# Kernel optimization log

Measured on AMD Instinct MI355X. Metric: run time of the kernel, lower is better.

## Reference

```python
import jax, jax.numpy as jnp
import numpy as np

# --- static config (matches init_kwargs) ---
DIM = 192          # kv channels
CS = 2             # channel_scale -> q/out channels = DIM//CS
NH = 6             # num heads
WS = 4             # kv window size (q window = 2*WS)
S, H, W = 16, 32, 32          # coarse (input) resolution
SD, HD, WD = 32, 64, 64
HEAD = DIM // NH
SCALE = HEAD ** -0.5

# Relative position index: query coords are the fine-grid positions mapped to
# coarse coords via repeat_interleave(2) (as in the original coords_s/h/w),
# key coords are the coarse window positions. (Original torch code contained a
# buggy 2D->3D port of the strided key subsample; this is the consistent 3D form.)
_r = np.repeat(np.arange(WS), 2)
qc = np.stack(np.meshgrid(_r, _r, _r, indexing='ij'), -1).reshape(-1, 3)        # (512,3)
_k = np.arange(WS)
kc = np.stack(np.meshgrid(_k, _k, _k, indexing='ij'), -1).reshape(-1, 3)        # (64,3)
_rel = qc[:, None, :] - kc[None, :, :] + (WS - 1)                                # in [0, 2*WS-2]
REL_INDEX = jnp.asarray(_rel[..., 0] * (2 * WS - 1) ** 2 + _rel[..., 1] * (2 * WS - 1) + _rel[..., 2])  # (512,64)
TABLE_ROWS = (4 * WS - 1) ** 3  # as in original parameter shape


def ln(x, g, b, eps=1e-5):
    mu = jnp.mean(x, axis=-1, keepdims=True)
    var = jnp.mean(jnp.square(x - mu), axis=-1, keepdims=True)
    return (x - mu) * jax.lax.rsqrt(var + eps) * g + b


def win_part(x, ws):
    # (B,s,h,w,C) -> (B*num_windows, ws^3, C)
    B, s, h, w, C = x.shape
    x = x.reshape(B, s // ws, ws, h // ws, ws, w // ws, ws, C)
    return x.transpose(0, 1, 3, 5, 2, 4, 6, 7).reshape(-1, ws * ws * ws, C)


def win_rev(x, ws, B, s, h, w):
    # (B*num_windows, ws^3, C) -> (B,s,h,w,C)
    C = x.shape[-1]
    x = x.reshape(B, s // ws, h // ws, w // ws, ws, ws, ws, C)
    return x.transpose(0, 1, 4, 2, 5, 3, 6, 7).reshape(B, s, h, w, C)


def setup_inputs() -> dict:
    key = jax.random.key(0)
    ks = jax.random.split(key, 12)
    d = DIM
    dh = d // CS
    hid = int(dh * 4)
    f = lambda i, shape: jax.random.normal(ks[i], shape, jnp.float32) * 0.02
    return dict(
        x=jax.random.normal(ks[0], (2, S * H * W, d), jnp.float32),
        x_downsampled=jax.random.normal(ks[1], (2, SD * HD * WD, dh), jnp.float32),
        gamma1=jnp.ones((d,), jnp.float32), beta1=jnp.zeros((d,), jnp.float32),
        W_kv=f(2, (d, 2 * d)), b_kv=jnp.zeros((2 * d,), jnp.float32),
        W_q=f(3, (dh, d)), b_q=jnp.zeros((d,), jnp.float32),
        W_proj=f(4, (d, dh)), b_proj=jnp.zeros((dh,), jnp.float32),
        bias_table=f(5, (TABLE_ROWS, NH)),
        exp_gamma=jnp.ones((d,), jnp.float32), exp_beta=jnp.zeros((d,), jnp.float32),
        deconv_w=f(6, (d, dh, 2, 2, 2)), deconv_b=jnp.zeros((dh,), jnp.float32),
        gamma2=jnp.ones((dh,), jnp.float32), beta2=jnp.zeros((dh,), jnp.float32),
        W1=f(7, (dh, hid)), b1=jnp.zeros((hid,), jnp.float32),
        W2=f(8, (hid, dh)), b2=jnp.zeros((dh,), jnp.float32),
        padwh=0,
    )


def reference(x, x_downsampled, gamma1, beta1, W_kv, b_kv, W_q, b_q, W_proj, b_proj,
              bias_table, exp_gamma, exp_beta, deconv_w, deconv_b, gamma2, beta2,
              W1, b1, W2, b2, padwh):
    B = x.shape[0]
    d = DIM
    dh = d // CS
    # ---- windowed cross attention: kv from coarse x (norm1), q from fine skip ----
    kv = ln(x, gamma1, beta1).reshape(B, S, H, W, d)
    kv_w = win_part(kv, WS)                                           # (Bw, 64, d)
    q_w = win_part(x_downsampled.reshape(B, SD, HD, WD, dh), 2 * WS)  # (Bw, 512, dh)
    Bw, N, _ = kv_w.shape
    Nq = q_w.shape[1]
    kvp = kv_w @ W_kv + b_kv                                          # (Bw, N, 2d)
    k, v = jnp.split(kvp, 2, axis=-1)
    k = k.reshape(Bw, N, NH, HEAD).transpose(0, 2, 1, 3)
    v = v.reshape(Bw, N, NH, HEAD).transpose(0, 2, 1, 3)
    q = (q_w @ W_q + b_q).reshape(Bw, Nq, NH, HEAD).transpose(0, 2, 1, 3) * SCALE
    attn = jnp.einsum('bhqd,bhkd->bhqk', q, k)                        # (Bw, NH, 512, 64)
    bias = bias_table[REL_INDEX].transpose(2, 0, 1)                   # (NH, 512, 64)
    attn = jax.nn.softmax(attn + bias[None], axis=-1)
    out = jnp.einsum('bhqk,bhkd->bhqd', attn, v).transpose(0, 2, 1, 3).reshape(Bw, Nq, d)
    out = out @ W_proj + b_proj                                       # (Bw, Nq, dh)
    out = win_rev(out, 2 * WS, B, SD, HD, WD).reshape(B, SD * HD * WD, dh)
    # ---- Patch_Expanding residual: LN + ConvTranspose3d(k=2, s=2) ----
    xe = ln(x, exp_gamma, exp_beta).reshape(B, S, H, W, d)
    sc = jnp.einsum('bshwc,coijk->bsihjwko', xe, deconv_w) + deconv_b  # (B,S,2,H,2,W,2,dh)
    sc = sc.reshape(B, SD * HD * WD, dh)
    # ---- residual + MLP ----
    y = sc + out
    hdn = jax.nn.gelu(ln(y, gamma2, beta2) @ W1 + b1, approximate=False)
    return y + (hdn @ W2 + b2)
```

## Files before the change

### kernel.cpp

```cpp
#include <hip/hip_runtime.h>
#include <math.h>

#define ATT_SCALE 0.17677669529663687f

typedef __bf16 bf16x8 __attribute__((ext_vector_type(8)));
typedef __bf16 bf16x4 __attribute__((ext_vector_type(4)));
typedef float  f32x4  __attribute__((ext_vector_type(4)));

#define MFMA16(a,b,c) __builtin_amdgcn_mfma_f32_16x16x32_bf16(a,b,c,0,0,0)

#define BIAS_BYTES 786432
#define WKV_OFF 0
#define WQ_OFF  73728
#define WP_OFF  92160
#define WD_OFF  110592
#define W1_OFF  258048
#define W2_OFF  294912
#define NSWZ    331776

static __device__ __forceinline__ float gelu_exact(float v){
    return 0.5f * v * (1.0f + erff(v * 0.70710678118654752f));
}

static __device__ __forceinline__ bf16x8 afrag(const __bf16* w, int NRT, int kt, int rt, int lane){
    return ((const bf16x8*)w)[(kt*NRT + rt)*64 + lane];
}

__global__ __launch_bounds__(256) void k_prep(const float* __restrict__ table,
    const float* __restrict__ Wkv, const float* __restrict__ Wq,
    const float* __restrict__ Wp,  const float* __restrict__ Wd,
    const float* __restrict__ W1,  const float* __restrict__ W2,
    float* __restrict__ bias, __bf16* __restrict__ wsw){
    int id = blockIdx.x * 256 + threadIdx.x;
    if (id < 196608){
        int k  = id & 63;
        int qg = (id >> 6) & 511;
        int h  = id >> 15;
        int qi = qg >> 6, qj = (qg >> 3) & 7, qk = qg & 7;
        int ki = k >> 4,  kj = (k >> 2) & 3,  kk = k & 3;
        int r0 = (qi >> 1) - ki + 3;
        int r1 = (qj >> 1) - kj + 3;
        int r2 = (qk >> 1) - kk + 3;
        bias[id] = table[((r0 * 7 + r1) * 7 + r2) * 6 + h];
        return;
    }
    id -= 196608;
    if (id >= NSWZ) return;
    if (id >= WD_OFF && id < W1_OFF){
        int lid  = id - WD_OFF;
        int j    = lid & 7, lane = (lid >> 3) & 63, tile = lid >> 9;
        int rt   = tile % 24;
        int kt2  = tile / 24;
        int ii   = kt2 / 6, kt = kt2 % 6;
        int n    = rt * 16 + (lane & 15);
        int o    = n % 96, jk = n / 96;
        int kdim = kt * 32 + (lane >> 4) * 8 + j;
        wsw[id] = (__bf16)(Wd[(kdim * 96 + o) * 8 + ii * 4 + jk]);
        return;
    }
    const float* W; int N, NRT, off; float sc = 1.f;
    if      (id < WQ_OFF){ W = Wkv; N = 384; NRT = 24; off = WKV_OFF; }
    else if (id < WP_OFF){ W = Wq;  N = 192; NRT = 12; off = WQ_OFF; sc = ATT_SCALE; }
    else if (id < WD_OFF){ W = Wp;  N = 96;  NRT = 6;  off = WP_OFF; }
    else if (id < W2_OFF){ W = W1;  N = 384; NRT = 24; off = W1_OFF; }
    else                 { W = W2;  N = 96;  NRT = 6;  off = W2_OFF; }
    int lid  = id - off;
    int j    = lid & 7, lane = (lid >> 3) & 63, tile = lid >> 9;
    int rt   = tile % NRT, kt = tile / NRT;
    int n    = rt * 16 + (lane & 15);
    int k    = kt * 32 + (lane >> 4) * 8 + j;
    wsw[id + 0] = (__bf16)(W[k * N + n] * sc);
}

__global__ __launch_bounds__(512) void k_deconv(const float* __restrict__ x,
    const float* __restrict__ eg, const float* __restrict__ eb,
    const __bf16* __restrict__ wsw, const float* __restrict__ db,
    float* __restrict__ out){
    __shared__ __bf16 xe[64][200];
    const int tid = threadIdx.x, lane = tid & 63, w = tid >> 6;
    const int ci0 = blockIdx.x * 64;
    {
        int row = tid >> 3, sub = tid & 7;
        const float* xp = x + (ci0 + row) * 192 + sub * 24;
        float v[24]; float s = 0.f, ss = 0.f;
        #pragma unroll
        for (int i = 0; i < 6; i++){
            float4 t = ((const float4*)xp)[i];
            v[4*i] = t.x; v[4*i+1] = t.y; v[4*i+2] = t.z; v[4*i+3] = t.w;
            s += t.x + t.y + t.z + t.w;
            ss += t.x*t.x + t.y*t.y + t.z*t.z + t.w*t.w;
        }
        #pragma unroll
        for (int m = 1; m < 8; m <<= 1){ s += __shfl_xor(s, m); ss += __shfl_xor(ss, m); }
        float mu = s * (1.f/192.f), var = ss * (1.f/192.f) - mu*mu, rs = rsqrtf(var + 1e-5f);
        #pragma unroll
        for (int i = 0; i < 3; i++){
            bf16x8 t;
            #pragma unroll
            for (int jj = 0; jj < 8; jj++){
                int c = sub*24 + 8*i + jj;
                t[jj] = (__bf16)((v[8*i+jj] - mu) * rs * eg[c] + eb[c]);
            }
            *(bf16x8*)&xe[row][sub*24 + 8*i] = t;
        }
    }
    __syncthreads();
    const int li = lane & 15, gt = lane >> 4;
    const int ct = w & 3, ii = w >> 2;
    const int tok = ct * 16 + li;
    const int ci  = ci0 + tok;
    const int bb  = ci >> 14, rem = ci & 16383;
    const int sC  = rem >> 10, hC = (rem >> 5) & 31, wC = rem & 31;
    const int ftb = ((bb * 32 + 2 * sC) * 64 + 2 * hC) * 64 + 2 * wC + ii * 4096;
    bf16x8 bfr[6];
    #pragma unroll
    for (int kt = 0; kt < 6; kt++) bfr[kt] = *(const bf16x8*)&xe[tok][kt*32 + gt*8];
    const __bf16* wd = wsw + WD_OFF + ii * 73728;
    for (int rt = 0; rt < 24; rt++){
        f32x4 acc = {0.f,0.f,0.f,0.f};
        #pragma unroll
        for (int kt = 0; kt < 6; kt++) acc = MFMA16(afrag(wd, 24, kt, rt, lane), bfr[kt], acc);
        int m  = rt * 16 + (gt << 2);
        int jk = m / 96, o = m - jk * 96;
        int ft = ftb + (jk >> 1) * 64 + (jk & 1);
        float4 d4 = *(const float4*)&db[o];
        float4 res;
        res.x = acc[0] + d4.x; res.y = acc[1] + d4.y;
        res.z = acc[2] + d4.z; res.w = acc[3] + d4.w;
        *(float4*)&out[ft * 96 + o] = res;
    }
}

__global__ __launch_bounds__(512) void k_attn(const float* __restrict__ x,
    const float* __restrict__ xd, const float* __restrict__ g1, const float* __restrict__ b1v,
    const float* __restrict__ bkv, const float* __restrict__ bq, const float* __restrict__ bpj,
    const __bf16* __restrict__ wsw, const float* __restrict__ bias, float* __restrict__ yout){
    __shared__ __bf16 Qs[64][196];
    __shared__ __bf16 Os[64][196];
    __shared__ __bf16 Ks[64][196];
    __shared__ __bf16 Vt[192][68];
    const int tid = threadIdx.x, lane = tid & 63, w = tid >> 6;
    const int win = blockIdx.x, b = win >> 8, wrem = win & 255;
    const int sw_ = wrem >> 6, hw_ = (wrem >> 3) & 7, ww_ = wrem & 7;

    {
        int row = tid >> 3, sub = tid & 7;
        int si = row >> 4, hi = (row >> 2) & 3, wi = row & 3;
        int ci = ((b * 16 + 4 * sw_ + si) * 32 + 4 * hw_ + hi) * 32 + 4 * ww_ + wi;
        const float* xp = x + ci * 192 + sub * 24;
        float v[24]; float s = 0.f, ss = 0.f;
        #pragma unroll
        for (int i = 0; i < 6; i++){
            float4 t = ((const float4*)xp)[i];
            v[4*i] = t.x; v[4*i+1] = t.y; v[4*i+2] = t.z; v[4*i+3] = t.w;
            s += t.x + t.y + t.z + t.w;
            ss += t.x*t.x + t.y*t.y + t.z*t.z + t.w*t.w;
        }
        #pragma unroll
        for (int m = 1; m < 8; m <<= 1){ s += __shfl_xor(s, m); ss += __shfl_xor(ss, m); }
        float mu = s * (1.f/192.f), var = ss * (1.f/192.f) - mu*mu, rs = rsqrtf(var + 1e-5f);
        #pragma unroll
        for (int i = 0; i < 3; i++){
            bf16x8 t;
            #pragma unroll
            for (int jj = 0; jj < 8; jj++){
                int c = sub*24 + 8*i + jj;
                t[jj] = (__bf16)((v[8*i+jj] - mu) * rs * g1[c] + b1v[c]);
            }
            *(bf16x8*)&Qs[row][sub*24 + 8*i] = t;
        }
    }
    __syncthreads();
    {
        const int ct = w & 3, rh = w >> 2;
        const int tok = ct * 16 + (lane & 15);
        bf16x8 bfr[6];
        #pragma unroll
        for (int kt = 0; kt < 6; kt++) bfr[kt] = *(const bf16x8*)&Qs[tok][kt*32 + (lane>>4)*8];
        #pragma unroll
        for (int i = 0; i < 12; i++){
            int rt = rh * 12 + i;
            f32x4 acc = {0.f,0.f,0.f,0.f};
            #pragma unroll
            for (int kt = 0; kt < 6; kt++) acc = MFMA16(afrag(wsw + WKV_OFF, 24, kt, rt, lane), bfr[kt], acc);
            int cb = rt * 16 + ((lane >> 4) << 2);
            float4 b4 = *(const float4*)&bkv[cb];
            acc[0] += b4.x; acc[1] += b4.y; acc[2] += b4.z; acc[3] += b4.w;
            if (cb < 192){
                bf16x4 t;
                #pragma unroll
                for (int r = 0; r < 4; r++) t[r] = (__bf16)acc[r];
                *(bf16x4*)&Ks[tok][cb] = t;
            } else {
                #pragma unroll
                for (int r = 0; r < 4; r++) Vt[cb - 192 + r][tok] = (__bf16)acc[r];
            }
        }
    }
    __syncthreads();

    const int li_ = lane & 15, gt_ = lane >> 4, rsel = lane >> 5;
    const int ctQ = w & 3, rhQ = w >> 2;
    const int qlQ = ctQ * 16 + li_;

    auto qproj = [&](int qt){
        const int ft = ((b * 32 + 8 * sw_ + qt) * 64 + 8 * hw_ + (qlQ >> 3)) * 64 + 8 * ww_ + (qlQ & 7);
        bf16x8 bfr[3];
        #pragma unroll
        for (int kt = 0; kt < 3; kt++){
            const float* xp = xd + ft * 96 + kt * 32 + gt_ * 8;
            float4 t0 = *(const float4*)xp;
            float4 t1 = *(const float4*)(xp + 4);
            bf16x8 t;
            t[0]=(__bf16)t0.x; t[1]=(__bf16)t0.y; t[2]=(__bf16)t0.z; t[3]=(__bf16)t0.w;
            t[4]=(__bf16)t1.x; t[5]=(__bf16)t1.y; t[6]=(__bf16)t1.z; t[7]=(__bf16)t1.w;
            bfr[kt] = t;
        }
        #pragma unroll
        for (int i = 0; i < 6; i++){
            int rt = rhQ * 6 + i;
            f32x4 acc = {0.f,0.f,0.f,0.f};
            #pragma unroll
            for (int kt = 0; kt < 3; kt++) acc = MFMA16(afrag(wsw + WQ_OFF, 12, kt, rt, lane), bfr[kt], acc);
            int cb = rt * 16 + (gt_ << 2);
            float4 b4 = *(const float4*)&bq[cb];
            bf16x4 t;
            t[0] = (__bf16)(acc[0] + b4.x * ATT_SCALE);
            t[1] = (__bf16)(acc[1] + b4.y * ATT_SCALE);
            t[2] = (__bf16)(acc[2] + b4.z * ATT_SCALE);
            t[3] = (__bf16)(acc[3] + b4.w * ATT_SCALE);
            *(bf16x4*)&Qs[qlQ][cb] = t;
        }
    };

    auto outproj = [&](int qt){
        const int ft = ((b * 32 + 8 * sw_ + qt) * 64 + 8 * hw_ + (qlQ >> 3)) * 64 + 8 * ww_ + (qlQ & 7);
        bf16x8 bfr[6];
        #pragma unroll
        for (int kt = 0; kt < 6; kt++) bfr[kt] = *(const bf16x8*)&Os[qlQ][kt*32 + gt_*8];
        #pragma unroll
        for (int i = 0; i < 3; i++){
            int rt = rhQ * 3 + i;
            f32x4 acc = {0.f,0.f,0.f,0.f};
            #pragma unroll
            for (int kt = 0; kt < 6; kt++) acc = MFMA16(afrag(wsw + WP_OFF, 6, kt, rt, lane), bfr[kt], acc);
            int cb = rt * 16 + (gt_ << 2);
            float4 b4 = *(const float4*)&bpj[cb];
            float4 old = *(const float4*)&yout[ft * 96 + cb];
            float4 res;
            res.x = old.x + acc[0] + b4.x;
            res.y = old.y + acc[1] + b4.y;
            res.z = old.z + acc[2] + b4.z;
            res.w = old.w + acc[3] + b4.w;
            *(float4*)&yout[ft * 96 + cb] = res;
        }
    };

    qproj(0);
    __syncthreads();

    for (int qt = 0; qt < 8; qt++){
        #pragma unroll
        for (int ui = 0; ui < 3; ui++){
            const int u = w * 3 + ui;
            const int h = u >> 2, qct = u & 3;
            f32x4 sc[4];
            __builtin_amdgcn_s_setprio(1);
            #pragma unroll
            for (int rt = 0; rt < 4; rt++){
                bf16x8 a  = *(const bf16x8*)&Ks[rt*16 + li_][h*32 + gt_*8];
                bf16x8 bq8 = *(const bf16x8*)&Qs[qct*16 + li_][h*32 + gt_*8];
                f32x4 z = {0.f,0.f,0.f,0.f};
                sc[rt] = MFMA16(a, bq8, z);
            }
            __builtin_amdgcn_s_setprio(0);
            const int qg = qt * 64 + qct * 16 + li_;
            const float* bp = bias + (h * 512 + qg) * 64 + (gt_ << 2);
            #pragma unroll
            for (int rt = 0; rt < 4; rt++){
                float4 b4 = *(const float4*)(bp + rt * 16);
                sc[rt][0] += b4.x; sc[rt][1] += b4.y; sc[rt][2] += b4.z; sc[rt][3] += b4.w;
            }
            float m = sc[0][0];
            #pragma unroll
            for (int rt = 0; rt < 4; rt++)
                #pragma unroll
                for (int r = 0; r < 4; r++) m = fmaxf(m, sc[rt][r]);
            m = fmaxf(m, __shfl_xor(m, 16));
            m = fmaxf(m, __shfl_xor(m, 32));
            float sum = 0.f;
            #pragma unroll
            for (int rt = 0; rt < 4; rt++)
                #pragma unroll
                for (int r = 0; r < 4; r++){ float e = __expf(sc[rt][r] - m); sc[rt][r] = e; sum += e; }
            sum += __shfl_xor(sum, 16);
            sum += __shfl_xor(sum, 32);
            float inv = 1.f / sum;
            unsigned pwv[4][2];
            #pragma unroll
            for (int rt = 0; rt < 4; rt++){
                union { __bf16 hh[2]; unsigned u; } c0, c1;
                c0.hh[0] = (__bf16)(sc[rt][0] * inv); c0.hh[1] = (__bf16)(sc[rt][1] * inv);
                c1.hh[0] = (__bf16)(sc[rt][2] * inv); c1.hh[1] = (__bf16)(sc[rt][3] * inv);
                pwv[rt][0] = c0.u; pwv[rt][1] = c1.u;
            }
            unsigned bfw[2][4];
            #pragma unroll
            for (int kt = 0; kt < 2; kt++){
                #pragma unroll
                for (int t = 0; t < 4; t++){
                    int gs   = ((gt_ & 1) << 1) + (t >> 1);
                    int addr = (((gs << 4) + li_) << 2);
                    int w0 = __builtin_amdgcn_ds_bpermute(addr, (int)pwv[2*kt + 0][t & 1]);
                    int w1 = __builtin_amdgcn_ds_bpermute(addr, (int)pwv[2*kt + 1][t & 1]);
                    bfw[kt][t] = rsel ? (unsigned)w1 : (unsigned)w0;
                }
            }
            union { unsigned u[4]; bf16x8 v; } pb0, pb1;
            #pragma unroll
            for (int t = 0; t < 4; t++){ pb0.u[t] = bfw[0][t]; pb1.u[t] = bfw[1][t]; }
            __builtin_amdgcn_s_setprio(1);
            #pragma unroll
            for (int dt = 0; dt < 2; dt++){
                f32x4 o = {0.f,0.f,0.f,0.f};
                bf16x8 a0 = *(const bf16x8*)&Vt[h*32 + dt*16 + li_][gt_*8];
                bf16x8 a1 = *(const bf16x8*)&Vt[h*32 + dt*16 + li_][32 + gt_*8];
                o = MFMA16(a0, pb0.v, o);
                o = MFMA16(a1, pb1.v, o);
                const int tok = qct * 16 + li_;
                int cb = h * 32 + dt * 16 + (gt_ << 2);
                bf16x4 t;
                #pragma unroll
                for (int r = 0; r < 4; r++) t[r] = (__bf16)o[r];
                *(bf16x4*)&Os[tok][cb] = t;
            }
            __builtin_amdgcn_s_setprio(0);
        }
        __syncthreads();
        outproj(qt);
        if (qt < 7) qproj(qt + 1);
        __syncthreads();
    }
}

__global__ __launch_bounds__(512) void k_mlp(const float* __restrict__ y,
    const float* __restrict__ g2, const float* __restrict__ b2v,
    const __bf16* __restrict__ wsw, const float* __restrict__ b1m,
    const float* __restrict__ b2m, float* __restrict__ outp){
    __shared__ __bf16 yln[64][104];
    __shared__ __bf16 hsm[64][200];
    __shared__ __bf16 ybf[64][96];
    const int tid = threadIdx.x, lane = tid & 63, w = tid >> 6;
    const int t0 = blockIdx.x * 64;
    {
        int row = tid >> 3, sub = tid & 7;
        const float* yp = y + (t0 + row) * 96 + sub * 12;
        float v[12]; float s = 0.f, ss = 0.f;
        #pragma unroll
        for (int i = 0; i < 3; i++){
            float4 t = ((const float4*)yp)[i];
            v[4*i] = t.x; v[4*i+1] = t.y; v[4*i+2] = t.z; v[4*i+3] = t.w;
            s += t.x + t.y + t.z + t.w;
            ss += t.x*t.x + t.y*t.y + t.z*t.z + t.w*t.w;
        }
        #pragma unroll
        for (int i = 0; i < 3; i++){
            bf16x4 t;
            #pragma unroll
            for (int jj = 0; jj < 4; jj++) t[jj] = (__bf16)v[4*i+jj];
            *(bf16x4*)&ybf[row][sub*12 + 4*i] = t;
        }
        #pragma unroll
        for (int m = 1; m < 8; m <<= 1){ s += __shfl_xor(s, m); ss += __shfl_xor(ss, m); }
        float mu = s * (1.f/96.f), var = ss * (1.f/96.f) - mu*mu, rs = rsqrtf(var + 1e-5f);
        #pragma unroll
        for (int i = 0; i < 3; i++){
            bf16x4 t;
            #pragma unroll
            for (int jj = 0; jj < 4; jj++){
                int c = sub*12 + 4*i + jj;
                t[jj] = (__bf16)((v[4*i+jj] - mu) * rs * g2[c] + b2v[c]);
            }
            *(bf16x4*)&yln[row][sub*12 + 4*i] = t;
        }
    }
    __syncthreads();
    const int ct = w & 3, rh = w >> 2;
    const int tok = ct * 16 + (lane & 15);
    bf16x8 bfrY[3];
    #pragma unroll
    for (int kt = 0; kt < 3; kt++) bfrY[kt] = *(const bf16x8*)&yln[tok][kt*32 + (lane>>4)*8];
    f32x4 oacc[3];
    #pragma unroll
    for (int i = 0; i < 3; i++){ f32x4 z = {0.f,0.f,0.f,0.f}; oacc[i] = z; }

    #pragma unroll
    for (int hh = 0; hh < 2; hh++){
        #pragma unroll
        for (int i = 0; i < 6; i++){
            int rtl = rh * 6 + i;
            int rtg = hh * 12 + rtl;
            f32x4 acc = {0.f,0.f,0.f,0.f};
            #pragma unroll
            for (int kt = 0; kt < 3; kt++) acc = MFMA16(afrag(wsw + W1_OFF, 24, kt, rtg, lane), bfrY[kt], acc);
            int cb = rtl * 16 + ((lane >> 4) << 2);
            float4 b4 = *(const float4*)&b1m[hh * 192 + cb];
            bf16x4 t;
            t[0] = (__bf16)gelu_exact(acc[0] + b4.x);
            t[1] = (__bf16)gelu_exact(acc[1] + b4.y);
            t[2] = (__bf16)gelu_exact(acc[2] + b4.z);
            t[3] = (__bf16)gelu_exact(acc[3] + b4.w);
            *(bf16x4*)&hsm[tok][cb] = t;
        }
        __syncthreads();
        bf16x8 bfrH[6];
        #pragma unroll
        for (int kt = 0; kt < 6; kt++) bfrH[kt] = *(const bf16x8*)&hsm[tok][kt*32 + (lane>>4)*8];
        #pragma unroll
        for (int i = 0; i < 3; i++){
            int rt = rh * 3 + i;
            #pragma unroll
            for (int kt = 0; kt < 6; kt++)
                oacc[i] = MFMA16(afrag(wsw + W2_OFF, 6, hh * 6 + kt, rt, lane), bfrH[kt], oacc[i]);
        }
        __syncthreads();
    }
    #pragma unroll
    for (int i = 0; i < 3; i++){
        int rt = rh * 3 + i;
        int cb = rt * 16 + ((lane >> 4) << 2);
        float4 b4 = *(const float4*)&b2m[cb];
        bf16x4 yv = *(const bf16x4*)&ybf[tok][cb];
        float4 res;
        res.x = (float)yv[0] + oacc[i][0] + b4.x;
        res.y = (float)yv[1] + oacc[i][1] + b4.y;
        res.z = (float)yv[2] + oacc[i][2] + b4.z;
        res.w = (float)yv[3] + oacc[i][3] + b4.w;
        *(float4*)&outp[(t0 + tok) * 96 + cb] = res;
    }
}

extern "C" void kernel_launch(void* const* d_in, const int* in_sizes, int n_in,
                              void* d_out, int out_size, void* d_ws, size_t ws_size,
                              hipStream_t stream){
    const float* x    = (const float*)d_in[0];
    const float* xd   = (const float*)d_in[1];
    const float* g1   = (const float*)d_in[2];
    const float* b1v  = (const float*)d_in[3];
    const float* Wkv  = (const float*)d_in[4];
    const float* bkv  = (const float*)d_in[5];
    const float* Wq   = (const float*)d_in[6];
    const float* bq   = (const float*)d_in[7];
    const float* Wp   = (const float*)d_in[8];
    const float* bpj  = (const float*)d_in[9];
    const float* btab = (const float*)d_in[10];
    const float* eg   = (const float*)d_in[11];
    const float* eb   = (const float*)d_in[12];
    const float* dw   = (const float*)d_in[13];
    const float* db   = (const float*)d_in[14];
    const float* g2   = (const float*)d_in[15];
    const float* b2v  = (const float*)d_in[16];
    const float* W1   = (const float*)d_in[17];
    const float* b1m  = (const float*)d_in[18];
    const float* W2   = (const float*)d_in[19];
    const float* b2m  = (const float*)d_in[20];
    (void)in_sizes; (void)n_in; (void)out_size; (void)ws_size;

    float*   out  = (float*)d_out;
    float*   bias = (float*)d_ws;
    __bf16*  wsw  = (__bf16*)((char*)d_ws + BIAS_BYTES);

    k_prep  <<<2064, 256, 0, stream>>>(btab, Wkv, Wq, Wp, dw, W1, W2, bias, wsw);
    k_deconv<<<512, 512, 0, stream>>>(x, eg, eb, wsw, db, out);
    k_attn  <<<512, 512, 0, stream>>>(x, xd, g1, b1v, bkv, bq, bpj, wsw, bias, out);
    k_mlp   <<<4096, 512, 0, stream>>>(out, g2, b2v, wsw, b1m, b2m, out);
}
```

Baseline: 328.4 us.

## Process two attention windows per block in k_attn with halved grid

Each attention block now handles two windows, so the grid shrinks from 512 to 256 blocks. Q, K and V shared buffers are doubled and the separate O buffer is dropped. Attention outputs are kept in registers and then written back into the Q buffer, which adds an extra barrier per q-tile. The aim is to get more independent work per wave to hide latency and to amortise weight-fragment loads across two windows. In exchange it uses more LDS and registers and puts only 256 blocks on the 256-CU MI355X, which may lower occupancy and parallelism.

```diff
diff --git a/kernel.cpp b/kernel.cpp
--- a/kernel.cpp
+++ b/kernel.cpp
@@ -135,18 +135,25 @@
     const float* __restrict__ xd, const float* __restrict__ g1, const float* __restrict__ b1v,
     const float* __restrict__ bkv, const float* __restrict__ bq, const float* __restrict__ bpj,
     const __bf16* __restrict__ wsw, const float* __restrict__ bias, float* __restrict__ yout){
-    __shared__ __bf16 Qs[64][196];
-    __shared__ __bf16 Os[64][196];
-    __shared__ __bf16 Ks[64][196];
-    __shared__ __bf16 Vt[192][68];
+    __shared__ __bf16 Qs[2][64][196];
+    __shared__ __bf16 Ks[2][64][196];
+    __shared__ __bf16 Vt[2][192][68];
     const int tid = threadIdx.x, lane = tid & 63, w = tid >> 6;
-    const int win = blockIdx.x, b = win >> 8, wrem = win & 255;
-    const int sw_ = wrem >> 6, hw_ = (wrem >> 3) & 7, ww_ = wrem & 7;
-
-    {
+
+    int bW[2], swW[2], hwW[2], wwW[2];
+    #pragma unroll
+    for (int ws = 0; ws < 2; ws++){
+        int win = blockIdx.x * 2 + ws;
+        bW[ws] = win >> 8;
+        int wrem = win & 255;
+        swW[ws] = wrem >> 6; hwW[ws] = (wrem >> 3) & 7; wwW[ws] = wrem & 7;
+    }
+
+    #pragma unroll
+    for (int ws = 0; ws < 2; ws++){
         int row = tid >> 3, sub = tid & 7;
         int si = row >> 4, hi = (row >> 2) & 3, wi = row & 3;
-        int ci = ((b * 16 + 4 * sw_ + si) * 32 + 4 * hw_ + hi) * 32 + 4 * ww_ + wi;
+        int ci = ((bW[ws] * 16 + 4 * swW[ws] + si) * 32 + 4 * hwW[ws] + hi) * 32 + 4 * wwW[ws] + wi;
         const float* xp = x + ci * 192 + sub * 24;
         float v[24]; float s = 0.f, ss = 0.f;
         #pragma unroll
@@ -167,16 +174,17 @@
                 int c = sub*24 + 8*i + jj;
                 t[jj] = (__bf16)((v[8*i+jj] - mu) * rs * g1[c] + b1v[c]);
             }
-            *(bf16x8*)&Qs[row][sub*24 + 8*i] = t;
+            *(bf16x8*)&Qs[ws][row][sub*24 + 8*i] = t;
         }
     }
     __syncthreads();
-    {
+    #pragma unroll
+    for (int ws = 0; ws < 2; ws++){
         const int ct = w & 3, rh = w >> 2;
         const int tok = ct * 16 + (lane & 15);
         bf16x8 bfr[6];
         #pragma unroll
-        for (int kt = 0; kt < 6; kt++) bfr[kt] = *(const bf16x8*)&Qs[tok][kt*32 + (lane>>4)*8];
+        for (int kt = 0; kt < 6; kt++) bfr[kt] = *(const bf16x8*)&Qs[ws][tok][kt*32 + (lane>>4)*8];
         #pragma unroll
         for (int i = 0; i < 12; i++){
             int rt = rh * 12 + i;
@@ -190,10 +198,10 @@
                 bf16x4 t;
                 #pragma unroll
                 for (int r = 0; r < 4; r++) t[r] = (__bf16)acc[r];
-                *(bf16x4*)&Ks[tok][cb] = t;
+                *(bf16x4*)&Ks[ws][tok][cb] = t;
             } else {
                 #pragma unroll
-                for (int r = 0; r < 4; r++) Vt[cb - 192 + r][tok] = (__bf16)acc[r];
+                for (int r = 0; r < 4; r++) Vt[ws][cb - 192 + r][tok] = (__bf16)acc[r];
             }
         }
     }
@@ -203,142 +211,155 @@
     const int ctQ = w & 3, rhQ = w >> 2;
     const int qlQ = ctQ * 16 + li_;
 
-    auto qproj = [&](int qt){
-        const int ft = ((b * 32 + 8 * sw_ + qt) * 64 + 8 * hw_ + (qlQ >> 3)) * 64 + 8 * ww_ + (qlQ & 7);
-        bf16x8 bfr[3];
-        #pragma unroll
-        for (int kt = 0; kt < 3; kt++){
-            const float* xp = xd + ft * 96 + kt * 32 + gt_ * 8;
-            float4 t0 = *(const float4*)xp;
-            float4 t1 = *(const float4*)(xp + 4);
-            bf16x8 t;
-            t[0]=(__bf16)t0.x; t[1]=(__bf16)t0.y; t[2]=(__bf16)t0.z; t[3]=(__bf16)t0.w;
-            t[4]=(__bf16)t1.x; t[5]=(__bf16)t1.y; t[6]=(__bf16)t1.z; t[7]=(__bf16)t1.w;
-            bfr[kt] = t;
-        }
-        #pragma unroll
-        for (int i = 0; i < 6; i++){
-            int rt = rhQ * 6 + i;
-            f32x4 acc = {0.f,0.f,0.f,0.f};
-            #pragma unroll
-            for (int kt = 0; kt < 3; kt++) acc = MFMA16(afrag(wsw + WQ_OFF, 12, kt, rt, lane), bfr[kt], acc);
-            int cb = rt * 16 + (gt_ << 2);
-            float4 b4 = *(const float4*)&bq[cb];
-            bf16x4 t;
-            t[0] = (__bf16)(acc[0] + b4.x * ATT_SCALE);
-            t[1] = (__bf16)(acc[1] + b4.y * ATT_SCALE);
-            t[2] = (__bf16)(acc[2] + b4.z * ATT_SCALE);
-            t[3] = (__bf16)(acc[3] + b4.w * ATT_SCALE);
-            *(bf16x4*)&Qs[qlQ][cb] = t;
-        }
-    };
-
-    auto outproj = [&](int qt){
-        const int ft = ((b * 32 + 8 * sw_ + qt) * 64 + 8 * hw_ + (qlQ >> 3)) * 64 + 8 * ww_ + (qlQ & 7);
-        bf16x8 bfr[6];
-        #pragma unroll
-        for (int kt = 0; kt < 6; kt++) bfr[kt] = *(const bf16x8*)&Os[qlQ][kt*32 + gt_*8];
-        #pragma unroll
-        for (int i = 0; i < 3; i++){
-            int rt = rhQ * 3 + i;
-            f32x4 acc = {0.f,0.f,0.f,0.f};
-            #pragma unroll
-            for (int kt = 0; kt < 6; kt++) acc = MFMA16(afrag(wsw + WP_OFF, 6, kt, rt, lane), bfr[kt], acc);
-            int cb = rt * 16 + (gt_ << 2);
-            float4 b4 = *(const float4*)&bpj[cb];
-            float4 old = *(const float4*)&yout[ft * 96 + cb];
-            float4 res;
-            res.x = old.x + acc[0] + b4.x;
-            res.y = old.y + acc[1] + b4.y;
-            res.z = old.z + acc[2] + b4.z;
-            res.w = old.w + acc[3] + b4.w;
-            *(float4*)&yout[ft * 96 + cb] = res;
-        }
-    };
-
-    qproj(0);
-    __syncthreads();
-
     for (int qt = 0; qt < 8; qt++){
         #pragma unroll
-        for (int ui = 0; ui < 3; ui++){
-            const int u = w * 3 + ui;
-            const int h = u >> 2, qct = u & 3;
-            f32x4 sc[4];
-            __builtin_amdgcn_s_setprio(1);
-            #pragma unroll
-            for (int rt = 0; rt < 4; rt++){
-                bf16x8 a  = *(const bf16x8*)&Ks[rt*16 + li_][h*32 + gt_*8];
-                bf16x8 bq8 = *(const bf16x8*)&Qs[qct*16 + li_][h*32 + gt_*8];
-                f32x4 z = {0.f,0.f,0.f,0.f};
-                sc[rt] = MFMA16(a, bq8, z);
-            }
-            __builtin_amdgcn_s_setprio(0);
-            const int qg = qt * 64 + qct * 16 + li_;
-            const float* bp = bias + (h * 512 + qg) * 64 + (gt_ << 2);
-            #pragma unroll
-            for (int rt = 0; rt < 4; rt++){
-                float4 b4 = *(const float4*)(bp + rt * 16);
-                sc[rt][0] += b4.x; sc[rt][1] += b4.y; sc[rt][2] += b4.z; sc[rt][3] += b4.w;
-            }
-            float m = sc[0][0];
-            #pragma unroll
-            for (int rt = 0; rt < 4; rt++)
-                #pragma unroll
-                for (int r = 0; r < 4; r++) m = fmaxf(m, sc[rt][r]);
-            m = fmaxf(m, __shfl_xor(m, 16));
-            m = fmaxf(m, __shfl_xor(m, 32));
-            float sum = 0.f;
-            #pragma unroll
-            for (int rt = 0; rt < 4; rt++)
-                #pragma unroll
-                for (int r = 0; r < 4; r++){ float e = __expf(sc[rt][r] - m); sc[rt][r] = e; sum += e; }
-            sum += __shfl_xor(sum, 16);
-            sum += __shfl_xor(sum, 32);
-            float inv = 1.f / sum;
-            unsigned pwv[4][2];
-            #pragma unroll
-            for (int rt = 0; rt < 4; rt++){
-                union { __bf16 hh[2]; unsigned u; } c0, c1;
-                c0.hh[0] = (__bf16)(sc[rt][0] * inv); c0.hh[1] = (__bf16)(sc[rt][1] * inv);
-                c1.hh[0] = (__bf16)(sc[rt][2] * inv); c1.hh[1] = (__bf16)(sc[rt][3] * inv);
-                pwv[rt][0] = c0.u; pwv[rt][1] = c1.u;
-            }
-            unsigned bfw[2][4];
-            #pragma unroll
-            for (int kt = 0; kt < 2; kt++){
-                #pragma unroll
-                for (int t = 0; t < 4; t++){
-                    int gs   = ((gt_ & 1) << 1) + (t >> 1);
-                    int addr = (((gs << 4) + li_) << 2);
-                    int w0 = __builtin_amdgcn_ds_bpermute(addr, (int)pwv[2*kt + 0][t & 1]);
-                    int w1 = __builtin_amdgcn_ds_bpermute(addr, (int)pwv[2*kt + 1][t & 1]);
-                    bfw[kt][t] = rsel ? (unsigned)w1 : (unsigned)w0;
-                }
-            }
-            union { unsigned u[4]; bf16x8 v; } pb0, pb1;
-            #pragma unroll
-            for (int t = 0; t < 4; t++){ pb0.u[t] = bfw[0][t]; pb1.u[t] = bfw[1][t]; }
-            __builtin_amdgcn_s_setprio(1);
-            #pragma unroll
-            for (int dt = 0; dt < 2; dt++){
-                f32x4 o = {0.f,0.f,0.f,0.f};
-                bf16x8 a0 = *(const bf16x8*)&Vt[h*32 + dt*16 + li_][gt_*8];
-                bf16x8 a1 = *(const bf16x8*)&Vt[h*32 + dt*16 + li_][32 + gt_*8];
-                o = MFMA16(a0, pb0.v, o);
-                o = MFMA16(a1, pb1.v, o);
+        for (int ws = 0; ws < 2; ws++){
+            const int ft = ((bW[ws] * 32 + 8 * swW[ws] + qt) * 64 + 8 * hwW[ws] + (qlQ >> 3)) * 64 + 8 * wwW[ws] + (qlQ & 7);
+            bf16x8 bfr[3];
+            #pragma unroll
+            for (int kt = 0; kt < 3; kt++){
+                const float* xp = xd + ft * 96 + kt * 32 + gt_ * 8;
+                float4 t0 = *(const float4*)xp;
+                float4 t1 = *(const float4*)(xp + 4);
+                bf16x8 t;
+                t[0]=(__bf16)t0.x; t[1]=(__bf16)t0.y; t[2]=(__bf16)t0.z; t[3]=(__bf16)t0.w;
+                t[4]=(__bf16)t1.x; t[5]=(__bf16)t1.y; t[6]=(__bf16)t1.z; t[7]=(__bf16)t1.w;
+                bfr[kt] = t;
+            }
+            #pragma unroll
+            for (int i = 0; i < 6; i++){
+                int rt = rhQ * 6 + i;
+                f32x4 acc = {0.f,0.f,0.f,0.f};
+                #pragma unroll
+                for (int kt = 0; kt < 3; kt++) acc = MFMA16(afrag(wsw + WQ_OFF, 12, kt, rt, lane), bfr[kt], acc);
+                int cb = rt * 16 + (gt_ << 2);
+                float4 b4 = *(const float4*)&bq[cb];
+                bf16x4 t;
+                t[0] = (__bf16)(acc[0] + b4.x * ATT_SCALE);
+                t[1] = (__bf16)(acc[1] + b4.y * ATT_SCALE);
+                t[2] = (__bf16)(acc[2] + b4.z * ATT_SCALE);
+                t[3] = (__bf16)(acc[3] + b4.w * ATT_SCALE);
+                *(bf16x4*)&Qs[ws][qlQ][cb] = t;
+            }
+        }
+        __syncthreads();
+        f32x4 ov[2][3][2];
+        #pragma unroll
+        for (int ws = 0; ws < 2; ws++){
+            #pragma unroll
+            for (int ui = 0; ui < 3; ui++){
+                const int u = w * 3 + ui;
+                const int h = u >> 2, qct = u & 3;
+                f32x4 sc[4];
+                __builtin_amdgcn_s_setprio(1);
+                #pragma unroll
+                for (int rt = 0; rt < 4; rt++){
+                    bf16x8 a  = *(const bf16x8*)&Ks[ws][rt*16 + li_][h*32 + gt_*8];
+                    bf16x8 bq8 = *(const bf16x8*)&Qs[ws][qct*16 + li_][h*32 + gt_*8];
+                    f32x4 z = {0.f,0.f,0.f,0.f};
+                    sc[rt] = MFMA16(a, bq8, z);
+                }
+                __builtin_amdgcn_s_setprio(0);
+                const int qg = qt * 64 + qct * 16 + li_;
+                const float* bp = bias + (h * 512 + qg) * 64 + (gt_ << 2);
+                #pragma unroll
+                for (int rt = 0; rt < 4; rt++){
+                    float4 b4 = *(const float4*)(bp + rt * 16);
+                    sc[rt][0] += b4.x; sc[rt][1] += b4.y; sc[rt][2] += b4.z; sc[rt][3] += b4.w;
+                }
+                float m = sc[0][0];
+                #pragma unroll
+                for (int rt = 0; rt < 4; rt++)
+                    #pragma unroll
+                    for (int r = 0; r < 4; r++) m = fmaxf(m, sc[rt][r]);
+                m = fmaxf(m, __shfl_xor(m, 16));
+                m = fmaxf(m, __shfl_xor(m, 32));
+                float sum = 0.f;
+                #pragma unroll
+                for (int rt = 0; rt < 4; rt++)
+                    #pragma unroll
+                    for (int r = 0; r < 4; r++){ float e = __expf(sc[rt][r] - m); sc[rt][r] = e; sum += e; }
+                sum += __shfl_xor(sum, 16);
+                sum += __shfl_xor(sum, 32);
+                float inv = 1.f / sum;
+                unsigned pwv[4][2];
+                #pragma unroll
+                for (int rt = 0; rt < 4; rt++){
+                    union { __bf16 hh[2]; unsigned u; } c0, c1;
+                    c0.hh[0] = (__bf16)(sc[rt][0] * inv); c0.hh[1] = (__bf16)(sc[rt][1] * inv);
+                    c1.hh[0] = (__bf16)(sc[rt][2] * inv); c1.hh[1] = (__bf16)(sc[rt][3] * inv);
+                    pwv[rt][0] = c0.u; pwv[rt][1] = c1.u;
+                }
+                unsigned bfw[2][4];
+                #pragma unroll
+                for (int kt = 0; kt < 2; kt++){
+                    #pragma unroll
+                    for (int t = 0; t < 4; t++){
+                        int gs   = ((gt_ & 1) << 1) + (t >> 1);
+                        int addr = (((gs << 4) + li_) << 2);
+                        int w0 = __builtin_amdgcn_ds_bpermute(addr, (int)pwv[2*kt + 0][t & 1]);
+                        int w1 = __builtin_amdgcn_ds_bpermute(addr, (int)pwv[2*kt + 1][t & 1]);
+                        bfw[kt][t] = rsel ? (unsigned)w1 : (unsigned)w0;
+                    }
+                }
+                union { unsigned u[4]; bf16x8 v; } pb0, pb1;
+                #pragma unroll
+                for (int t = 0; t < 4; t++){ pb0.u[t] = bfw[0][t]; pb1.u[t] = bfw[1][t]; }
+                __builtin_amdgcn_s_setprio(1);
+                #pragma unroll
+                for (int dt = 0; dt < 2; dt++){
+                    f32x4 o = {0.f,0.f,0.f,0.f};
+                    bf16x8 a0 = *(const bf16x8*)&Vt[ws][h*32 + dt*16 + li_][gt_*8];
+                    bf16x8 a1 = *(const bf16x8*)&Vt[ws][h*32 + dt*16 + li_][32 + gt_*8];
+                    o = MFMA16(a0, pb0.v, o);
+                    o = MFMA16(a1, pb1.v, o);
+                    ov[ws][ui][dt] = o;
+                }
+                __builtin_amdgcn_s_setprio(0);
+            }
+        }
+        __syncthreads();
+        #pragma unroll
+        for (int ws = 0; ws < 2; ws++){
+            #pragma unroll
+            for (int ui = 0; ui < 3; ui++){
+                const int u = w * 3 + ui;
+                const int h = u >> 2, qct = u & 3;
                 const int tok = qct * 16 + li_;
-                int cb = h * 32 + dt * 16 + (gt_ << 2);
-                bf16x4 t;
-                #pragma unroll
-                for (int r = 0; r < 4; r++) t[r] = (__bf16)o[r];
-                *(bf16x4*)&Os[tok][cb] = t;
-            }
-            __builtin_amdgcn_s_setprio(0);
-        }
-        __syncthreads();
-        outproj(qt);
-        if (qt < 7) qproj(qt + 1);
+                #pragma unroll
+                for (int dt = 0; dt < 2; dt++){
+                    int cb = h * 32 + dt * 16 + (gt_ << 2);
+                    bf16x4 t;
+                    #pragma unroll
+                    for (int r = 0; r < 4; r++) t[r] = (__bf16)ov[ws][ui][dt][r];
+                    *(bf16x4*)&Qs[ws][tok][cb] = t;
+                }
+            }
+        }
+        __syncthreads();
+        #pragma unroll
+        for (int ws = 0; ws < 2; ws++){
+            const int ft = ((bW[ws] * 32 + 8 * swW[ws] + qt) * 64 + 8 * hwW[ws] + (qlQ >> 3)) * 64 + 8 * wwW[ws] + (qlQ & 7);
+            bf16x8 bfr[6];
+            #pragma unroll
+            for (int kt = 0; kt < 6; kt++) bfr[kt] = *(const bf16x8*)&Qs[ws][qlQ][kt*32 + gt_*8];
+            #pragma unroll
+            for (int i = 0; i < 3; i++){
+                int rt = rhQ * 3 + i;
+                f32x4 acc = {0.f,0.f,0.f,0.f};
+                #pragma unroll
+                for (int kt = 0; kt < 6; kt++) acc = MFMA16(afrag(wsw + WP_OFF, 6, kt, rt, lane), bfr[kt], acc);
+                int cb = rt * 16 + (gt_ << 2);
+                float4 b4 = *(const float4*)&bpj[cb];
+                float4 old = *(const float4*)&yout[ft * 96 + cb];
+                float4 res;
+                res.x = old.x + acc[0] + b4.x;
+                res.y = old.y + acc[1] + b4.y;
+                res.z = old.z + acc[2] + b4.z;
+                res.w = old.w + acc[3] + b4.w;
+                *(float4*)&yout[ft * 96 + cb] = res;
+            }
+        }
         __syncthreads();
     }
 }
@@ -472,6 +493,6 @@
 
     k_prep  <<<2064, 256, 0, stream>>>(btab, Wkv, Wq, Wp, dw, W1, W2, bias, wsw);
     k_deconv<<<512, 512, 0, stream>>>(x, eg, eb, wsw, db, out);
-    k_attn  <<<512, 512, 0, stream>>>(x, xd, g1, b1v, bkv, bq, bpj, wsw, bias, out);
+    k_attn  <<<256, 512, 0, stream>>>(x, xd, g1, b1v, bkv, bq, bpj, wsw, bias, out);
     k_mlp   <<<4096, 512, 0, stream>>>(out, g2, b2v, wsw, b1m, b2m, out);
 }
```

Result: slower. 461.9 us (+40.6%).
